# Performance work log

Hardware: AMD Instinct MI355X
Metric: run time of the kernel (lower is better)

## Reference

```python
import jax, jax.numpy as jnp
import numpy as np

N_NODES = 100000
N_EDGES = 800000
IN_DIM = 128
HID_DIM = 128


def setup_inputs() -> dict:
    key = jax.random.key(0)
    ks = jax.random.split(key, 10)
    s = 0.05
    return {
        "x": jax.random.normal(ks[0], (N_NODES, IN_DIM), dtype=jnp.float32),
        "edge_index": jax.random.randint(ks[1], (2, N_EDGES), 0, N_NODES, dtype=jnp.int64),
        "W1l": jax.random.normal(ks[2], (HID_DIM, IN_DIM), dtype=jnp.float32) * s,
        "b1": jax.random.normal(ks[3], (HID_DIM,), dtype=jnp.float32) * s,
        "W1r": jax.random.normal(ks[4], (HID_DIM, IN_DIM), dtype=jnp.float32) * s,
        "W2l": jax.random.normal(ks[5], (HID_DIM, HID_DIM), dtype=jnp.float32) * s,
        "b2": jax.random.normal(ks[6], (HID_DIM,), dtype=jnp.float32) * s,
        "W2r": jax.random.normal(ks[7], (HID_DIM, HID_DIM), dtype=jnp.float32) * s,
        "Wfc": jax.random.normal(ks[8], (1, HID_DIM), dtype=jnp.float32) * s,
        "bfc": jax.random.normal(ks[9], (1,), dtype=jnp.float32) * s,
    }


def _sage_conv(h, src, dst, n_nodes, Wl, b, Wr):
    # PyG SAGEConv (mean aggr): lin_l(mean_{j in N(i)} x_j) + lin_r(x_i)
    msg = h[src]  # [E, D] gather from source nodes
    agg = jax.ops.segment_sum(msg, dst, num_segments=n_nodes)  # [N, D]
    cnt = jax.ops.segment_sum(jnp.ones((src.shape[0], 1), h.dtype), dst,
                              num_segments=n_nodes)  # [N, 1]
    mean = agg / jnp.maximum(cnt, 1.0)  # isolated nodes -> 0 (matches scatter-mean)
    return mean @ Wl.T + b + h @ Wr.T


def reference(x, edge_index, W1l, b1, W1r, W2l, b2, W2r, Wfc, bfc):
    src, dst = edge_index[0], edge_index[1]
    n = x.shape[0]
    h = jax.nn.relu(_sage_conv(x, src, dst, n, W1l, b1, W1r))
    h = jax.nn.relu(_sage_conv(h, src, dst, n, W2l, b2, W2r))
    # dropout is identity in eval mode
    out = h @ Wfc.T + bfc  # [N, 1]
    return out.squeeze(-1)  # [N]
```

## Files before the change

### kernel.cpp

```cpp
#include <hip/hip_runtime.h>

#define N_NODES 100000
#define N_EDGES 800000
#define DIM 128

#define NB 391
#define BKCAP 2560
#define EPB 2048
#define BINB ((N_EDGES + EPB - 1) / EPB)

typedef __attribute__((ext_vector_type(8))) short short8;
typedef __attribute__((ext_vector_type(4))) float float4v;
typedef __attribute__((ext_vector_type(2))) float float2v;
typedef __attribute__((ext_vector_type(4))) unsigned int uint4v;

__device__ __forceinline__ float lo16(unsigned int v) {
    return __uint_as_float(v << 16);
}
__device__ __forceinline__ float hi16(unsigned int v) {
    return __uint_as_float(v & 0xffff0000u);
}
__device__ __forceinline__ float2v unp(unsigned int v) {
    return (float2v){lo16(v), hi16(v)};
}
__device__ __forceinline__ unsigned short f2bf(float f) {
    unsigned int x = __float_as_uint(f);
    unsigned int r = x + 0x7fffu + ((x >> 16) & 1u);
    return (unsigned short)(r >> 16);
}
__device__ __forceinline__ unsigned int packbf(float a, float b) {
    return (unsigned int)f2bf(a) | ((unsigned int)f2bf(b) << 16);
}


__global__ void edet_kernel(const int* __restrict__ edge, int* __restrict__ flags,
                            int* __restrict__ cur) {
    int i = blockIdx.x * blockDim.x + threadIdx.x;
    if (i < NB) cur[i] = 0;
    if (i < N_EDGES && edge[2 * i + 1] != 0) flags[1] = 1;
}


#define NXD (N_NODES * DIM / 2)

__global__ void conv_kernel(const float* __restrict__ x, const float* __restrict__ a,
                            const float* __restrict__ b, const float* __restrict__ c,
                            const float* __restrict__ d, unsigned int* __restrict__ xdst,
                            unsigned int* __restrict__ wdst) {
    int i = blockIdx.x * blockDim.x + threadIdx.x;
    if (i < NXD) {
        float2 v = ((const float2*)x)[i];
        xdst[i] = packbf(v.x, v.y);
    } else {
        int j = i - NXD;
        if (j < 4 * 8192) {
            int m = j >> 13, r = j & 8191;
            const float* src = (m == 0) ? a : (m == 1) ? b : (m == 2) ? c : d;
            float2 v = ((const float2*)src)[r];
            wdst[j] = packbf(v.x, v.y);
        }
    }
}


__device__ __forceinline__ void load_edge(const int* __restrict__ edge, int eflag, int e,
                                          int& s, int& d) {
    if (eflag == 0) {
        s = edge[2 * e];
        d = edge[2 * (N_EDGES + e)];
    } else {
        s = edge[e];
        d = edge[N_EDGES + e];
    }
}

__global__ __launch_bounds__(256) void bin_kernel(const int* __restrict__ edge,
                                                  const int* __restrict__ flags,
                                                  int* __restrict__ cur,
                                                  unsigned int* __restrict__ pairs) {
    __shared__ int lcnt[NB];
    __shared__ int lbase[NB];
    int t = threadIdx.x;
    for (int i = t; i < NB; i += 256) lcnt[i] = 0;
    __syncthreads();
    int e0 = blockIdx.x * EPB;
    int eflag = (flags[1] == 1) ? 1 : 0;
    int vb[8];
    unsigned int vp[8];
    bool valid[8];
#pragma unroll
    for (int k = 0; k < 8; ++k) {
        int e = e0 + k * 256 + t;
        valid[k] = false;
        if (e < N_EDGES) {
            int s, d;
            load_edge(edge, eflag, e, s, d);
            if ((unsigned)s < N_NODES && (unsigned)d < N_NODES) {
                valid[k] = true;
                vb[k] = d >> 8;
                vp[k] = ((unsigned int)s << 8) | (unsigned int)(d & 255);
                atomicAdd(&lcnt[vb[k]], 1);
            }
        }
    }
    __syncthreads();
    for (int i = t; i < NB; i += 256) {
        int c = lcnt[i];
        lbase[i] = (c > 0) ? atomicAdd(&cur[i], c) : 0;
        lcnt[i] = 0;
    }
    __syncthreads();
#pragma unroll
    for (int k = 0; k < 8; ++k) {
        if (valid[k]) {
            int b = vb[k];
            int pos = lbase[b] + atomicAdd(&lcnt[b], 1);
            if (pos < BKCAP)
                pairs[(size_t)b * BKCAP + pos] = vp[k];
        }
    }
}

__global__ __launch_bounds__(512) void bscan_kernel(const int* __restrict__ cur,
                                                    int* __restrict__ boff,
                                                    int* __restrict__ rowptr) {
    __shared__ int sh[512];
    int t = threadIdx.x;
    int v = (t < NB) ? min(cur[t], BKCAP) : 0;
    sh[t] = v;
    __syncthreads();
    for (int off = 1; off < 512; off <<= 1) {
        int u = 0;
        if (t >= off) u = sh[t - off];
        __syncthreads();
        if (t >= off) sh[t] += u;
        __syncthreads();
    }
    if (t < NB) boff[t] = sh[t] - v;
    if (t == 511) rowptr[N_NODES] = sh[511];
}

__global__ __launch_bounds__(256) void csr_kernel(const int* __restrict__ cur,
                                                  const int* __restrict__ boff,
                                                  const unsigned int* __restrict__ pairs,
                                                  int* __restrict__ rowptr,
                                                  int* __restrict__ esrc) {
    __shared__ int hist[256];
    __shared__ int lofs[256];
    __shared__ int nsh;
    int b = blockIdx.x, t = threadIdx.x;
    if (t == 0) nsh = min(cur[b], BKCAP);
    hist[t] = 0;
    __syncthreads();
    int n = nsh;
    const unsigned int* p = pairs + (size_t)b * BKCAP;
    for (int i = t; i < n; i += 256) atomicAdd(&hist[p[i] & 255u], 1);
    __syncthreads();
    int v = hist[t];
    lofs[t] = v;
    __syncthreads();
    for (int off = 1; off < 256; off <<= 1) {
        int u = 0;
        if (t >= off) u = lofs[t - off];
        __syncthreads();
        if (t >= off) lofs[t] += u;
        __syncthreads();
    }
    int excl = lofs[t] - v;
    int base = boff[b];
    int node = b * 256 + t;
    if (node < N_NODES) rowptr[node] = base + excl;
    __syncthreads();
    hist[t] = excl;
    __syncthreads();
    for (int i = t; i < n; i += 256) {
        unsigned int pk = p[i];
        int pos = atomicAdd(&hist[pk & 255u], 1);
        esrc[base + pos] = (int)(pk >> 8);
    }
}


__global__ __launch_bounds__(256) void agg_kernel(const unsigned int* __restrict__ feat2,
                                                  const int* __restrict__ rowptr,
                                                  const int* __restrict__ esrc,
                                                  unsigned int* __restrict__ meanout) {
    int node = (blockIdx.x * blockDim.x + threadIdx.x) >> 6;
    int lane = threadIdx.x & 63;
    if (node >= N_NODES) return;
    int rowgrp = lane >> 4;
    int dimgrp = lane & 15;
    int beg = rowptr[node], end = rowptr[node + 1];
    float2v a0 = {0.f, 0.f}, a1 = {0.f, 0.f}, a2 = {0.f, 0.f}, a3 = {0.f, 0.f};
    int e = beg;
    for (; e + 8 <= end; e += 8) {
        int s0 = esrc[e + rowgrp];
        int s1 = esrc[e + 4 + rowgrp];
        uint4v v0 = *(const uint4v*)(feat2 + (size_t)s0 * 64 + dimgrp * 4);
        uint4v v1 = *(const uint4v*)(feat2 + (size_t)s1 * 64 + dimgrp * 4);
        a0 += unp(v0.x) + unp(v1.x);
        a1 += unp(v0.y) + unp(v1.y);
        a2 += unp(v0.z) + unp(v1.z);
        a3 += unp(v0.w) + unp(v1.w);
    }
    for (; e < end; e += 4) {
        int idx = e + rowgrp;
        bool ok = idx < end;
        int s = esrc[ok ? idx : end - 1];
        uint4v v = *(const uint4v*)(feat2 + (size_t)s * 64 + dimgrp * 4);
        float2v m = {ok ? 1.f : 0.f, ok ? 1.f : 0.f};
        a0 += m * unp(v.x);
        a1 += m * unp(v.y);
        a2 += m * unp(v.z);
        a3 += m * unp(v.w);
    }
    a0.x += __shfl_xor(a0.x, 16, 64); a0.x += __shfl_xor(a0.x, 32, 64);
    a0.y += __shfl_xor(a0.y, 16, 64); a0.y += __shfl_xor(a0.y, 32, 64);
    a1.x += __shfl_xor(a1.x, 16, 64); a1.x += __shfl_xor(a1.x, 32, 64);
    a1.y += __shfl_xor(a1.y, 16, 64); a1.y += __shfl_xor(a1.y, 32, 64);
    a2.x += __shfl_xor(a2.x, 16, 64); a2.x += __shfl_xor(a2.x, 32, 64);
    a2.y += __shfl_xor(a2.y, 16, 64); a2.y += __shfl_xor(a2.y, 32, 64);
    a3.x += __shfl_xor(a3.x, 16, 64); a3.x += __shfl_xor(a3.x, 32, 64);
    a3.y += __shfl_xor(a3.y, 16, 64); a3.y += __shfl_xor(a3.y, 32, 64);
    int deg = end - beg;
    float sc = deg > 0 ? 1.f / (float)deg : 0.f;
    float2v sel = (rowgrp == 0) ? a0 : (rowgrp == 1) ? a1 : (rowgrp == 2) ? a2 : a3;
    meanout[(size_t)node * 64 + dimgrp * 4 + rowgrp] = packbf(sel.x * sc, sel.y * sc);
}


template <int FUSE_FC>
__global__ __launch_bounds__(256, 2) void gemm_kernel(
    const unsigned short* __restrict__ A0, const unsigned short* __restrict__ A1,
    const unsigned int* __restrict__ Wpk,
    const float* __restrict__ bias, const float* __restrict__ wfc,
    const float* __restrict__ bfc, unsigned short* __restrict__ hout,
    float* __restrict__ out) {
    __shared__ unsigned int wlds[16384];

    {
        int mat = threadIdx.x >> 7, row = threadIdx.x & 127;
        const unsigned int* g = Wpk + mat * 8192 + row * 64;
        unsigned int* lbase = wlds + mat * 8192;
#pragma unroll
        for (int q = 0; q < 16; ++q) {
            uint4v v = *(const uint4v*)(g + q * 4);
            *(uint4v*)(lbase + ((q * 128 + row) << 2)) = v;
        }
    }
    __syncthreads();

    int wave = threadIdx.x >> 6;
    int lane = threadIdx.x & 63;
    int lrow = lane & 15;
    int qsel = lane >> 4;
    int rowBase = blockIdx.x * 256 + wave * 64;

    float4v acc[4][8];
#pragma unroll
    for (int mt = 0; mt < 4; ++mt)
#pragma unroll
        for (int nt = 0; nt < 8; ++nt) acc[mt][nt] = (float4v){0.f, 0.f, 0.f, 0.f};

    const unsigned short* Ah[2] = {A0, A1};
    int r4a[4];
#pragma unroll
    for (int mt = 0; mt < 4; ++mt) {
        int r = rowBase + mt * 16 + lrow;
        r4a[mt] = (r >= N_NODES) ? (N_NODES - 1) : r;
    }

    short8 a[2][4];
    {
#pragma unroll
        for (int mt = 0; mt < 4; ++mt) {
            a[0][mt] = *(const short8*)(A0 + (size_t)r4a[mt] * DIM + qsel * 8);
            a[1][mt] = *(const short8*)(A0 + (size_t)r4a[mt] * DIM + 32 + qsel * 8);
        }
    }

#pragma unroll
    for (int step = 0; step < 8; ++step) {
        int half = step >> 2, kt = step & 3;
        short8 cur[4];
#pragma unroll
        for (int mt = 0; mt < 4; ++mt) cur[mt] = a[step & 1][mt];
        if (step < 6) {
            int ns = step + 2;
            int nk0 = (ns & 3) * 32 + qsel * 8;
            const unsigned short* A = Ah[ns >> 2];
#pragma unroll
            for (int mt = 0; mt < 4; ++mt)
                a[step & 1][mt] = *(const short8*)(A + (size_t)r4a[mt] * DIM + nk0);
        }
        const unsigned int* lbase = wlds + half * 8192;
        int qg = kt * 4 + qsel;
#pragma unroll
        for (int nt = 0; nt < 8; ++nt) {
            short8 b = *(const short8*)(lbase + ((qg * 128 + nt * 16 + lrow) << 2));
#pragma unroll
            for (int mt = 0; mt < 4; ++mt)
                acc[mt][nt] = __builtin_amdgcn_mfma_f32_16x16x32_bf16(cur[mt], b, acc[mt][nt], 0, 0, 0);
        }
    }

    int crow0 = (lane >> 4) * 4;
    if (!FUSE_FC) {
#pragma unroll
        for (int mt = 0; mt < 4; ++mt) {
#pragma unroll
            for (int nt = 0; nt < 8; ++nt) {
                int col = nt * 16 + lrow;
                float bv = bias[col];
#pragma unroll
                for (int r4 = 0; r4 < 4; ++r4) {
                    int row = rowBase + mt * 16 + crow0 + r4;
                    if (row < N_NODES) {
                        float v = acc[mt][nt][r4] + bv;
                        hout[(size_t)row * DIM + col] = f2bf(v > 0.f ? v : 0.f);
                    }
                }
            }
        }
    } else {
        float bv[8], wv[8];
#pragma unroll
        for (int nt = 0; nt < 8; ++nt) {
            bv[nt] = bias[nt * 16 + lrow];
            wv[nt] = wfc[nt * 16 + lrow];
        }
        float bf0 = bfc[0];
#pragma unroll
        for (int mt = 0; mt < 4; ++mt) {
#pragma unroll
            for (int r4 = 0; r4 < 4; ++r4) {
                float p = 0.f;
#pragma unroll
                for (int nt = 0; nt < 8; ++nt) {
                    float v = acc[mt][nt][r4] + bv[nt];
                    p += (v > 0.f ? v : 0.f) * wv[nt];
                }
#pragma unroll
                for (int off = 1; off < 16; off <<= 1) p += __shfl_xor(p, off, 64);
                int row = rowBase + mt * 16 + crow0 + r4;
                if (lrow == 0 && row < N_NODES) out[row] = p + bf0;
            }
        }
    }
}


extern "C" void kernel_launch(void* const* d_in, const int* in_sizes, int n_in,
                              void* d_out, int out_size, void* d_ws, size_t ws_size,
                              hipStream_t stream) {
    const float* x  = (const float*)d_in[0];
    const int* edge = (const int*)d_in[1];
    const float* W1l = (const float*)d_in[2];
    const float* b1  = (const float*)d_in[3];
    const float* W1r = (const float*)d_in[4];
    const float* W2l = (const float*)d_in[5];
    const float* b2  = (const float*)d_in[6];
    const float* W2r = (const float*)d_in[7];
    const float* Wfc = (const float*)d_in[8];
    const float* bfc = (const float*)d_in[9];
    float* out = (float*)d_out;

    char* ws = (char*)d_ws;
    size_t off = 0;
    int* flags  = (int*)(ws + off); off += 256;
    int* rowptr = (int*)(ws + off); off += ((size_t)N_NODES + 64) * 4;
    int* esrc   = (int*)(ws + off); off += (size_t)N_EDGES * 4;
    int* cur    = (int*)(ws + off); off += (size_t)NB * 4 + 256;
    int* boff   = (int*)(ws + off); off += (size_t)NB * 4 + 256;
    off = (off + 255) & ~(size_t)255;
    unsigned int* pairs = (unsigned int*)(ws + off); off += (size_t)NB * BKCAP * 4;
    off = (off + 255) & ~(size_t)255;
    unsigned int* wbf = (unsigned int*)(ws + off); off += 4 * 8192 * 4;
    off = (off + 255) & ~(size_t)255;
    unsigned short* xbf  = (unsigned short*)(ws + off); off += (size_t)N_NODES * DIM * 2;
    unsigned short* mean = (unsigned short*)(ws + off); off += (size_t)N_NODES * DIM * 2;
    unsigned short* h1   = (unsigned short*)(ws + off); off += (size_t)N_NODES * DIM * 2;

    const int eBlocks = (N_EDGES + 255) / 256;
    const int waveBlocks = N_NODES / 4;
    const int gemmBlocks = (N_NODES + 255) / 256;
    const int convBlocks = (NXD + 4 * 8192 + 255) / 256;

    edet_kernel<<<eBlocks, 256, 0, stream>>>(edge, flags, cur);
    bin_kernel<<<BINB, 256, 0, stream>>>(edge, flags, cur, pairs);
    bscan_kernel<<<1, 512, 0, stream>>>(cur, boff, rowptr);
    csr_kernel<<<NB, 256, 0, stream>>>(cur, boff, pairs, rowptr, esrc);

    conv_kernel<<<convBlocks, 256, 0, stream>>>(x, W1l, W1r, W2l, W2r,
                                                (unsigned int*)xbf, wbf);

    agg_kernel<<<waveBlocks, 256, 0, stream>>>((const unsigned int*)xbf, rowptr, esrc,
                                               (unsigned int*)mean);
    gemm_kernel<0><<<gemmBlocks, 256, 0, stream>>>(mean, xbf, wbf, b1, nullptr, nullptr,
                                                   h1, nullptr);
    agg_kernel<<<waveBlocks, 256, 0, stream>>>((const unsigned int*)h1, rowptr, esrc,
                                               (unsigned int*)mean);
    gemm_kernel<1><<<gemmBlocks, 256, 0, stream>>>(mean, h1, wbf + 2 * 8192, b2, Wfc, bfc,
                                                   nullptr, out);
}
```

Measured before the change: 255.8 us.

## Shrink GEMM tiles and LDS for occupancy, cheaper shuffle reduction, sample edge check

The GEMM now uses 128-row blocks with half the accumulators. Weights are staged one 32 KB half at a time in LDS instead of 64 KB at once, and launch bounds rise to 4 blocks per CU, so more waves can hide gather-load latency. The aggregation's cross-lane reduction becomes a butterfly transpose with half as many shuffles. The int32/int64 edge-format check now runs on 16 blocks and inspects only the first 4096 edges instead of all of them. The cost is an extra barrier and reloading weights per half, and the format check now relies on a sample.

```diff
diff --git a/kernel.cpp b/kernel.cpp
--- a/kernel.cpp
+++ b/kernel.cpp
@@ -37,7 +37,7 @@
                             int* __restrict__ cur) {
     int i = blockIdx.x * blockDim.x + threadIdx.x;
     if (i < NB) cur[i] = 0;
-    if (i < N_EDGES && edge[2 * i + 1] != 0) flags[1] = 1;
+    if (edge[2 * i + 1] != 0) flags[1] = 1;
 }
 
 
@@ -214,100 +214,103 @@
         a2 += m * unp(v.z);
         a3 += m * unp(v.w);
     }
-    a0.x += __shfl_xor(a0.x, 16, 64); a0.x += __shfl_xor(a0.x, 32, 64);
-    a0.y += __shfl_xor(a0.y, 16, 64); a0.y += __shfl_xor(a0.y, 32, 64);
-    a1.x += __shfl_xor(a1.x, 16, 64); a1.x += __shfl_xor(a1.x, 32, 64);
-    a1.y += __shfl_xor(a1.y, 16, 64); a1.y += __shfl_xor(a1.y, 32, 64);
-    a2.x += __shfl_xor(a2.x, 16, 64); a2.x += __shfl_xor(a2.x, 32, 64);
-    a2.y += __shfl_xor(a2.y, 16, 64); a2.y += __shfl_xor(a2.y, 32, 64);
-    a3.x += __shfl_xor(a3.x, 16, 64); a3.x += __shfl_xor(a3.x, 32, 64);
-    a3.y += __shfl_xor(a3.y, 16, 64); a3.y += __shfl_xor(a3.y, 32, 64);
+    float2v s0v = (rowgrp & 1) ? a0 : a1;
+    float2v k0v = (rowgrp & 1) ? a1 : a0;
+    float2v s2v = (rowgrp & 1) ? a2 : a3;
+    float2v k2v = (rowgrp & 1) ? a3 : a2;
+    k0v.x += __shfl_xor(s0v.x, 16, 64);
+    k0v.y += __shfl_xor(s0v.y, 16, 64);
+    k2v.x += __shfl_xor(s2v.x, 16, 64);
+    k2v.y += __shfl_xor(s2v.y, 16, 64);
+    float2v sv = (rowgrp & 2) ? k0v : k2v;
+    float2v kv = (rowgrp & 2) ? k2v : k0v;
+    kv.x += __shfl_xor(sv.x, 32, 64);
+    kv.y += __shfl_xor(sv.y, 32, 64);
     int deg = end - beg;
     float sc = deg > 0 ? 1.f / (float)deg : 0.f;
-    float2v sel = (rowgrp == 0) ? a0 : (rowgrp == 1) ? a1 : (rowgrp == 2) ? a2 : a3;
-    meanout[(size_t)node * 64 + dimgrp * 4 + rowgrp] = packbf(sel.x * sc, sel.y * sc);
+    meanout[(size_t)node * 64 + dimgrp * 4 + rowgrp] = packbf(kv.x * sc, kv.y * sc);
 }
 
 
 template <int FUSE_FC>
-__global__ __launch_bounds__(256, 2) void gemm_kernel(
+__global__ __launch_bounds__(256, 4) void gemm_kernel(
     const unsigned short* __restrict__ A0, const unsigned short* __restrict__ A1,
     const unsigned int* __restrict__ Wpk,
     const float* __restrict__ bias, const float* __restrict__ wfc,
     const float* __restrict__ bfc, unsigned short* __restrict__ hout,
     float* __restrict__ out) {
-    __shared__ unsigned int wlds[16384];
-
-    {
-        int mat = threadIdx.x >> 7, row = threadIdx.x & 127;
-        const unsigned int* g = Wpk + mat * 8192 + row * 64;
-        unsigned int* lbase = wlds + mat * 8192;
-#pragma unroll
-        for (int q = 0; q < 16; ++q) {
-            uint4v v = *(const uint4v*)(g + q * 4);
-            *(uint4v*)(lbase + ((q * 128 + row) << 2)) = v;
-        }
-    }
-    __syncthreads();
+    __shared__ unsigned int wlds[8192];
 
     int wave = threadIdx.x >> 6;
     int lane = threadIdx.x & 63;
     int lrow = lane & 15;
     int qsel = lane >> 4;
-    int rowBase = blockIdx.x * 256 + wave * 64;
-
-    float4v acc[4][8];
-#pragma unroll
-    for (int mt = 0; mt < 4; ++mt)
+    int rowBase = blockIdx.x * 128 + wave * 32;
+
+    float4v acc[2][8];
+#pragma unroll
+    for (int mt = 0; mt < 2; ++mt)
 #pragma unroll
         for (int nt = 0; nt < 8; ++nt) acc[mt][nt] = (float4v){0.f, 0.f, 0.f, 0.f};
 
     const unsigned short* Ah[2] = {A0, A1};
-    int r4a[4];
-#pragma unroll
-    for (int mt = 0; mt < 4; ++mt) {
+    int r2a[2];
+#pragma unroll
+    for (int mt = 0; mt < 2; ++mt) {
         int r = rowBase + mt * 16 + lrow;
-        r4a[mt] = (r >= N_NODES) ? (N_NODES - 1) : r;
-    }
-
-    short8 a[2][4];
-    {
-#pragma unroll
-        for (int mt = 0; mt < 4; ++mt) {
-            a[0][mt] = *(const short8*)(A0 + (size_t)r4a[mt] * DIM + qsel * 8);
-            a[1][mt] = *(const short8*)(A0 + (size_t)r4a[mt] * DIM + 32 + qsel * 8);
-        }
-    }
-
-#pragma unroll
-    for (int step = 0; step < 8; ++step) {
-        int half = step >> 2, kt = step & 3;
-        short8 cur[4];
-#pragma unroll
-        for (int mt = 0; mt < 4; ++mt) cur[mt] = a[step & 1][mt];
-        if (step < 6) {
-            int ns = step + 2;
-            int nk0 = (ns & 3) * 32 + qsel * 8;
-            const unsigned short* A = Ah[ns >> 2];
-#pragma unroll
-            for (int mt = 0; mt < 4; ++mt)
-                a[step & 1][mt] = *(const short8*)(A + (size_t)r4a[mt] * DIM + nk0);
-        }
-        const unsigned int* lbase = wlds + half * 8192;
-        int qg = kt * 4 + qsel;
-#pragma unroll
-        for (int nt = 0; nt < 8; ++nt) {
-            short8 b = *(const short8*)(lbase + ((qg * 128 + nt * 16 + lrow) << 2));
-#pragma unroll
-            for (int mt = 0; mt < 4; ++mt)
-                acc[mt][nt] = __builtin_amdgcn_mfma_f32_16x16x32_bf16(cur[mt], b, acc[mt][nt], 0, 0, 0);
+        r2a[mt] = (r >= N_NODES) ? (N_NODES - 1) : r;
+    }
+
+    short8 a[2][2];
+#pragma unroll
+    for (int mt = 0; mt < 2; ++mt) {
+        a[0][mt] = *(const short8*)(A0 + (size_t)r2a[mt] * DIM + qsel * 8);
+        a[1][mt] = *(const short8*)(A0 + (size_t)r2a[mt] * DIM + 32 + qsel * 8);
+    }
+
+#pragma unroll
+    for (int half = 0; half < 2; ++half) {
+        if (half) __syncthreads();
+        {
+            int row = threadIdx.x & 127;
+            int qo = (threadIdx.x >> 7) * 8;
+            const unsigned int* g = Wpk + half * 8192 + row * 64 + qo * 4;
+#pragma unroll
+            for (int q = 0; q < 8; ++q) {
+                uint4v v = *(const uint4v*)(g + q * 4);
+                *(uint4v*)(wlds + (((qo + q) * 128 + row) << 2)) = v;
+            }
+        }
+        __syncthreads();
+#pragma unroll
+        for (int kt = 0; kt < 4; ++kt) {
+            int step = half * 4 + kt;
+            short8 cur[2];
+#pragma unroll
+            for (int mt = 0; mt < 2; ++mt) cur[mt] = a[step & 1][mt];
+            if (step < 6) {
+                int ns = step + 2;
+                int nk0 = (ns & 3) * 32 + qsel * 8;
+                const unsigned short* A = Ah[ns >> 2];
+#pragma unroll
+                for (int mt = 0; mt < 2; ++mt)
+                    a[step & 1][mt] = *(const short8*)(A + (size_t)r2a[mt] * DIM + nk0);
+            }
+            int qg = kt * 4 + qsel;
+#pragma unroll
+            for (int nt = 0; nt < 8; ++nt) {
+                short8 b = *(const short8*)(wlds + ((qg * 128 + nt * 16 + lrow) << 2));
+#pragma unroll
+                for (int mt = 0; mt < 2; ++mt)
+                    acc[mt][nt] = __builtin_amdgcn_mfma_f32_16x16x32_bf16(cur[mt], b, acc[mt][nt], 0, 0, 0);
+            }
         }
     }
 
     int crow0 = (lane >> 4) * 4;
     if (!FUSE_FC) {
 #pragma unroll
-        for (int mt = 0; mt < 4; ++mt) {
+        for (int mt = 0; mt < 2; ++mt) {
 #pragma unroll
             for (int nt = 0; nt < 8; ++nt) {
                 int col = nt * 16 + lrow;
@@ -331,7 +334,7 @@
         }
         float bf0 = bfc[0];
 #pragma unroll
-        for (int mt = 0; mt < 4; ++mt) {
+        for (int mt = 0; mt < 2; ++mt) {
 #pragma unroll
             for (int r4 = 0; r4 < 4; ++r4) {
                 float p = 0.f;
@@ -381,12 +384,11 @@
     unsigned short* mean = (unsigned short*)(ws + off); off += (size_t)N_NODES * DIM * 2;
     unsigned short* h1   = (unsigned short*)(ws + off); off += (size_t)N_NODES * DIM * 2;
 
-    const int eBlocks = (N_EDGES + 255) / 256;
     const int waveBlocks = N_NODES / 4;
-    const int gemmBlocks = (N_NODES + 255) / 256;
+    const int gemmBlocks = (N_NODES + 127) / 128;
     const int convBlocks = (NXD + 4 * 8192 + 255) / 256;
 
-    edet_kernel<<<eBlocks, 256, 0, stream>>>(edge, flags, cur);
+    edet_kernel<<<16, 256, 0, stream>>>(edge, flags, cur);
     bin_kernel<<<BINB, 256, 0, stream>>>(edge, flags, cur, pairs);
     bscan_kernel<<<1, 512, 0, stream>>>(cur, boff, rowptr);
     csr_kernel<<<NB, 256, 0, stream>>>(cur, boff, pairs, rowptr, esrc);
```

Result: no change. 260.2 us (+1.7%).

## Fuse graph-build kernels, shrink edge-format detection, and cheapen agg reductions

Applied to the files above, without the earlier changes.

Merges the bf16 conversion into the binning kernel as extra blocks, folds the bucket-offset scan into each CSR block (every block redundantly scans the bucket counts), and cuts the edge-format detect kernel to 16 blocks, dropping two launches. The aggregation reduction replaces sixteen cross-lane shuffles with eight using a butterfly transpose-reduce. The cost is redundant scan work in every CSR block. Detection now samples only the first 4096 edges, which could misdetect the index layout for unusual inputs.

```diff
diff --git a/kernel.cpp b/kernel.cpp
--- a/kernel.cpp
+++ b/kernel.cpp
@@ -8,6 +8,7 @@
 #define BKCAP 2560
 #define EPB 2048
 #define BINB ((N_EDGES + EPB - 1) / EPB)
+#define NXD (N_NODES * DIM / 2)
 
 typedef __attribute__((ext_vector_type(8))) short short8;
 typedef __attribute__((ext_vector_type(4))) float float4v;
@@ -37,29 +38,7 @@
                             int* __restrict__ cur) {
     int i = blockIdx.x * blockDim.x + threadIdx.x;
     if (i < NB) cur[i] = 0;
-    if (i < N_EDGES && edge[2 * i + 1] != 0) flags[1] = 1;
-}
-
-
-#define NXD (N_NODES * DIM / 2)
-
-__global__ void conv_kernel(const float* __restrict__ x, const float* __restrict__ a,
-                            const float* __restrict__ b, const float* __restrict__ c,
-                            const float* __restrict__ d, unsigned int* __restrict__ xdst,
-                            unsigned int* __restrict__ wdst) {
-    int i = blockIdx.x * blockDim.x + threadIdx.x;
-    if (i < NXD) {
-        float2 v = ((const float2*)x)[i];
-        xdst[i] = packbf(v.x, v.y);
-    } else {
-        int j = i - NXD;
-        if (j < 4 * 8192) {
-            int m = j >> 13, r = j & 8191;
-            const float* src = (m == 0) ? a : (m == 1) ? b : (m == 2) ? c : d;
-            float2 v = ((const float2*)src)[r];
-            wdst[j] = packbf(v.x, v.y);
-        }
-    }
+    if (edge[2 * i + 1] != 0) flags[1] = 1;
 }
 
 
@@ -74,13 +53,32 @@
     }
 }
 
-__global__ __launch_bounds__(256) void bin_kernel(const int* __restrict__ edge,
-                                                  const int* __restrict__ flags,
-                                                  int* __restrict__ cur,
-                                                  unsigned int* __restrict__ pairs) {
+
+__global__ __launch_bounds__(256) void binconv_kernel(
+    const int* __restrict__ edge, const int* __restrict__ flags, int* __restrict__ cur,
+    unsigned int* __restrict__ pairs, const float* __restrict__ x,
+    const float* __restrict__ wa, const float* __restrict__ wb,
+    const float* __restrict__ wc, const float* __restrict__ wd,
+    unsigned int* __restrict__ xdst, unsigned int* __restrict__ wdst) {
+    int t = threadIdx.x;
+    if (blockIdx.x >= BINB) {
+        int i = (blockIdx.x - BINB) * 256 + t;
+        if (i < NXD) {
+            float2 v = ((const float2*)x)[i];
+            xdst[i] = packbf(v.x, v.y);
+        } else {
+            int j = i - NXD;
+            if (j < 4 * 8192) {
+                int m = j >> 13, r = j & 8191;
+                const float* src = (m == 0) ? wa : (m == 1) ? wb : (m == 2) ? wc : wd;
+                float2 v = ((const float2*)src)[r];
+                wdst[j] = packbf(v.x, v.y);
+            }
+        }
+        return;
+    }
     __shared__ int lcnt[NB];
     __shared__ int lbase[NB];
-    int t = threadIdx.x;
     for (int i = t; i < NB; i += 256) lcnt[i] = 0;
     __syncthreads();
     int e0 = blockIdx.x * EPB;
@@ -121,38 +119,34 @@
     }
 }
 
-__global__ __launch_bounds__(512) void bscan_kernel(const int* __restrict__ cur,
-                                                    int* __restrict__ boff,
-                                                    int* __restrict__ rowptr) {
-    __shared__ int sh[512];
-    int t = threadIdx.x;
-    int v = (t < NB) ? min(cur[t], BKCAP) : 0;
-    sh[t] = v;
-    __syncthreads();
-    for (int off = 1; off < 512; off <<= 1) {
-        int u = 0;
-        if (t >= off) u = sh[t - off];
-        __syncthreads();
-        if (t >= off) sh[t] += u;
-        __syncthreads();
-    }
-    if (t < NB) boff[t] = sh[t] - v;
-    if (t == 511) rowptr[N_NODES] = sh[511];
-}
 
 __global__ __launch_bounds__(256) void csr_kernel(const int* __restrict__ cur,
-                                                  const int* __restrict__ boff,
                                                   const unsigned int* __restrict__ pairs,
                                                   int* __restrict__ rowptr,
                                                   int* __restrict__ esrc) {
+    __shared__ int sh[512];
     __shared__ int hist[256];
     __shared__ int lofs[256];
-    __shared__ int nsh;
     int b = blockIdx.x, t = threadIdx.x;
-    if (t == 0) nsh = min(cur[b], BKCAP);
+    int v0 = (t < NB) ? min(cur[t], BKCAP) : 0;
+    int t2 = t + 256;
+    int v1 = (t2 < NB) ? min(cur[t2], BKCAP) : 0;
+    sh[t] = v0;
+    sh[t2] = v1;
+    __syncthreads();
+    for (int off = 1; off < 512; off <<= 1) {
+        int u0 = (t >= off) ? sh[t - off] : 0;
+        int u1 = (t2 >= off) ? sh[t2 - off] : 0;
+        __syncthreads();
+        if (t >= off) sh[t] += u0;
+        sh[t2] += u1;
+        __syncthreads();
+    }
+    int n = min(cur[b], BKCAP);
+    int base = sh[b] - n;
+    if (b == 0 && t == 0) rowptr[N_NODES] = sh[NB - 1];
     hist[t] = 0;
     __syncthreads();
-    int n = nsh;
     const unsigned int* p = pairs + (size_t)b * BKCAP;
     for (int i = t; i < n; i += 256) atomicAdd(&hist[p[i] & 255u], 1);
     __syncthreads();
@@ -160,14 +154,12 @@
     lofs[t] = v;
     __syncthreads();
     for (int off = 1; off < 256; off <<= 1) {
-        int u = 0;
-        if (t >= off) u = lofs[t - off];
+        int u = (t >= off) ? lofs[t - off] : 0;
         __syncthreads();
         if (t >= off) lofs[t] += u;
         __syncthreads();
     }
     int excl = lofs[t] - v;
-    int base = boff[b];
     int node = b * 256 + t;
     if (node < N_NODES) rowptr[node] = base + excl;
     __syncthreads();
@@ -214,18 +206,21 @@
         a2 += m * unp(v.z);
         a3 += m * unp(v.w);
     }
-    a0.x += __shfl_xor(a0.x, 16, 64); a0.x += __shfl_xor(a0.x, 32, 64);
-    a0.y += __shfl_xor(a0.y, 16, 64); a0.y += __shfl_xor(a0.y, 32, 64);
-    a1.x += __shfl_xor(a1.x, 16, 64); a1.x += __shfl_xor(a1.x, 32, 64);
-    a1.y += __shfl_xor(a1.y, 16, 64); a1.y += __shfl_xor(a1.y, 32, 64);
-    a2.x += __shfl_xor(a2.x, 16, 64); a2.x += __shfl_xor(a2.x, 32, 64);
-    a2.y += __shfl_xor(a2.y, 16, 64); a2.y += __shfl_xor(a2.y, 32, 64);
-    a3.x += __shfl_xor(a3.x, 16, 64); a3.x += __shfl_xor(a3.x, 32, 64);
-    a3.y += __shfl_xor(a3.y, 16, 64); a3.y += __shfl_xor(a3.y, 32, 64);
+    float2v s0v = (rowgrp & 1) ? a0 : a1;
+    float2v k0v = (rowgrp & 1) ? a1 : a0;
+    float2v s2v = (rowgrp & 1) ? a2 : a3;
+    float2v k2v = (rowgrp & 1) ? a3 : a2;
+    k0v.x += __shfl_xor(s0v.x, 16, 64);
+    k0v.y += __shfl_xor(s0v.y, 16, 64);
+    k2v.x += __shfl_xor(s2v.x, 16, 64);
+    k2v.y += __shfl_xor(s2v.y, 16, 64);
+    float2v sv = (rowgrp & 2) ? k0v : k2v;
+    float2v kv = (rowgrp & 2) ? k2v : k0v;
+    kv.x += __shfl_xor(sv.x, 32, 64);
+    kv.y += __shfl_xor(sv.y, 32, 64);
     int deg = end - beg;
     float sc = deg > 0 ? 1.f / (float)deg : 0.f;
-    float2v sel = (rowgrp == 0) ? a0 : (rowgrp == 1) ? a1 : (rowgrp == 2) ? a2 : a3;
-    meanout[(size_t)node * 64 + dimgrp * 4 + rowgrp] = packbf(sel.x * sc, sel.y * sc);
+    meanout[(size_t)node * 64 + dimgrp * 4 + rowgrp] = packbf(kv.x * sc, kv.y * sc);
 }
 
 
@@ -271,12 +266,10 @@
     }
 
     short8 a[2][4];
-    {
-#pragma unroll
-        for (int mt = 0; mt < 4; ++mt) {
-            a[0][mt] = *(const short8*)(A0 + (size_t)r4a[mt] * DIM + qsel * 8);
-            a[1][mt] = *(const short8*)(A0 + (size_t)r4a[mt] * DIM + 32 + qsel * 8);
-        }
+#pragma unroll
+    for (int mt = 0; mt < 4; ++mt) {
+        a[0][mt] = *(const short8*)(A0 + (size_t)r4a[mt] * DIM + qsel * 8);
+        a[1][mt] = *(const short8*)(A0 + (size_t)r4a[mt] * DIM + 32 + qsel * 8);
     }
 
 #pragma unroll
@@ -371,7 +364,6 @@
     int* rowptr = (int*)(ws + off); off += ((size_t)N_NODES + 64) * 4;
     int* esrc   = (int*)(ws + off); off += (size_t)N_EDGES * 4;
     int* cur    = (int*)(ws + off); off += (size_t)NB * 4 + 256;
-    int* boff   = (int*)(ws + off); off += (size_t)NB * 4 + 256;
     off = (off + 255) & ~(size_t)255;
     unsigned int* pairs = (unsigned int*)(ws + off); off += (size_t)NB * BKCAP * 4;
     off = (off + 255) & ~(size_t)255;
@@ -381,18 +373,15 @@
     unsigned short* mean = (unsigned short*)(ws + off); off += (size_t)N_NODES * DIM * 2;
     unsigned short* h1   = (unsigned short*)(ws + off); off += (size_t)N_NODES * DIM * 2;
 
-    const int eBlocks = (N_EDGES + 255) / 256;
     const int waveBlocks = N_NODES / 4;
     const int gemmBlocks = (N_NODES + 255) / 256;
     const int convBlocks = (NXD + 4 * 8192 + 255) / 256;
 
-    edet_kernel<<<eBlocks, 256, 0, stream>>>(edge, flags, cur);
-    bin_kernel<<<BINB, 256, 0, stream>>>(edge, flags, cur, pairs);
-    bscan_kernel<<<1, 512, 0, stream>>>(cur, boff, rowptr);
-    csr_kernel<<<NB, 256, 0, stream>>>(cur, boff, pairs, rowptr, esrc);
-
-    conv_kernel<<<convBlocks, 256, 0, stream>>>(x, W1l, W1r, W2l, W2r,
-                                                (unsigned int*)xbf, wbf);
+    edet_kernel<<<16, 256, 0, stream>>>(edge, flags, cur);
+    binconv_kernel<<<BINB + convBlocks, 256, 0, stream>>>(edge, flags, cur, pairs, x,
+                                                          W1l, W1r, W2l, W2r,
+                                                          (unsigned int*)xbf, wbf);
+    csr_kernel<<<NB, 256, 0, stream>>>(cur, pairs, rowptr, esrc);
 
     agg_kernel<<<waveBlocks, 256, 0, stream>>>((const unsigned int*)xbf, rowptr, esrc,
                                                (unsigned int*)mean);
```

Result: faster. 244.5 us (-4.4%).
